# Performance work log

Hardware: AMD Instinct MI355X
Metric: run time of the kernel (lower is better)

The kernel has to match this reference:

```python
import jax, jax.numpy as jnp
import numpy as np

B, T = 256, 128
DW = 768          # dim_word
DH = 768          # dim_hidden (must equal DW per broadcast in original code)
NC = 3            # num_classification
VOCAB = 50000
TVOCAB = 5000


def setup_inputs() -> dict:
    key = jax.random.key(0)
    ks = jax.random.split(key, 16)
    u = 1.0 / np.sqrt(DH)
    uni = lambda k, shape: jax.random.uniform(k, shape, jnp.float32, -u, u)
    inp = {
        'sent': jax.random.randint(ks[0], (B, T), 0, VOCAB),
        'target': jax.random.randint(ks[1], (B,), 0, TVOCAB),
        'lens': jnp.clip(jax.random.randint(ks[2], (B,), 0, T + 1), 1, T),
        'emb': jax.random.normal(ks[3], (VOCAB, DW), jnp.float32) * 0.1,
        'temb': jax.random.normal(ks[4], (TVOCAB, DW), jnp.float32) * 0.1,
        # LSTM cell params: input = cat(x_t, target_x) -> 2*DW
        'W_ih': uni(ks[5], (2 * DW, 4 * DH)),
        'W_hh': uni(ks[6], (DH, 4 * DH)),
        'b_lstm': uni(ks[7], (4 * DH,)),
        'Wh': uni(ks[8], (DH, DH)),
        'Wv': uni(ks[9], (DW, DW)),
        'w': uni(ks[10], (DH + DW,)),
        'Wp': uni(ks[11], (DH, DH)),
        'Wx': uni(ks[12], (DH, DH)),
        'W_lin': uni(ks[13], (DH, NC)),
        'b_lin': uni(ks[14], (NC,)),
    }
    return inp


def _forward(sent, target, lens, emb, temb, W_ih, W_hh, b_lstm, Wh, Wv, w, Wp, Wx, W_lin, b_lin):
    x = emb[sent]                      # [B, T, DW]
    tx = temb[target]                  # [B, DW]
    mask = (jnp.arange(T)[None, :] < lens[:, None]).astype(x.dtype)  # [B, T]

    def step(carry, ins):
        h, c = carry
        xt, mt = ins                   # [B, DW], [B]
        inp = jnp.concatenate([xt, tx], axis=-1)          # [B, 2*DW]
        gates = inp @ W_ih + h @ W_hh + b_lstm            # [B, 4*DH]
        i, f, g, o = jnp.split(gates, 4, axis=-1)
        c_new = jax.nn.sigmoid(f) * c + jax.nn.sigmoid(i) * jnp.tanh(g)
        h_new = jax.nn.sigmoid(o) * jnp.tanh(c_new)
        m = mt[:, None]
        h = m * h_new + (1.0 - m) * h   # mask blend (hold state past seq end)
        c = m * c_new + (1.0 - m) * c
        return (h, c), h

    h0 = jnp.zeros((x.shape[0], DH), x.dtype)
    c0 = jnp.zeros((x.shape[0], DH), x.dtype)
    xs = (jnp.swapaxes(x, 0, 1), mask.T)                 # time-major
    _, Hs = jax.lax.scan(step, (h0, c0), xs)
    H = jnp.swapaxes(Hs, 0, 1)                            # [B, T, DH]

    # attention: M = tanh([H Wh ; aspect Wv]); scores = M @ w, masked softmax
    aspect_proj = (tx @ Wv)[:, None, :]                   # [B, 1, DW] broadcast over T
    M = jnp.tanh(jnp.concatenate(
        [H @ Wh, jnp.broadcast_to(aspect_proj, H.shape)], axis=-1))  # [B, T, DH+DW]
    scores = M @ w                                        # [B, T]
    scores = jnp.where(mask > 0, scores, -1e9)
    alpha = jax.nn.softmax(scores, axis=-1)               # [B, T]
    r = jnp.einsum('bt,btd->bd', alpha, H)                # [B, DH]
    h_star = jnp.tanh(r @ Wp + H[:, -1, :] @ Wx)          # [B, DH]
    # dropout is identity in eval mode
    logit = h_star @ W_lin + b_lin                        # [B, NC]
    return logit


def reference(sent, target, lens, emb, temb, W_ih, W_hh, b_lstm, Wh, Wv, w, Wp, Wx, W_lin, b_lin):
    return _forward(sent, target, lens, emb, temb, W_ih, W_hh, b_lstm,
                    Wh, Wv, w, Wp, Wx, W_lin, b_lin)
```

## Files before the change

kernel.cpp:

```cpp
#include <hip/hip_runtime.h>
#include <stdint.h>

#define Bz 256
#define Tz 128
#define DWz 768
#define DHz 768
#define G4z 3072
#define NBLK 96
#define NGRID 256
#define VOCABz 50000

typedef __attribute__((ext_vector_type(8))) short short8;
typedef __attribute__((ext_vector_type(4))) float f32x4;
typedef __attribute__((ext_vector_type(4))) int i32x4;

__device__ __forceinline__ unsigned short f2bf(float x) {
    union { float f; unsigned int u; } v; v.f = x;
    unsigned int u = v.u;
    return (unsigned short)((u + 0x7fffu + ((u >> 16) & 1u)) >> 16);
}
__device__ __forceinline__ float bf2f(unsigned short h) {
    union { unsigned int u; float f; } v; v.u = ((unsigned int)h) << 16;
    return v.f;
}
__device__ __forceinline__ float fsigm(float x) {
    return __builtin_amdgcn_rcpf(1.0f + __builtin_amdgcn_exp2f(x * -1.4426950408889634f));
}
__device__ __forceinline__ float ftanh(float x) {
    x = fminf(fmaxf(x, -15.0f), 15.0f);
    float e = __builtin_amdgcn_exp2f(x * -2.8853900817779268f);
    return (1.0f - e) * __builtin_amdgcn_rcpf(1.0f + e);
}

__global__ void k_cvt4(const float* __restrict__ src, unsigned short* __restrict__ dst, int n4) {
    int i = blockIdx.x * blockDim.x + threadIdx.x;
    int st = gridDim.x * blockDim.x;
    for (; i < n4; i += st) {
        float4 v = ((const float4*)src)[i];
        ushort4 o;
        o.x = f2bf(v.x); o.y = f2bf(v.y); o.z = f2bf(v.z); o.w = f2bf(v.w);
        ((ushort4*)dst)[i] = o;
    }
}

__global__ void k_prep_tx(const int* __restrict__ target, const float* __restrict__ temb,
                          float* __restrict__ tx) {
    int b = blockIdx.x;
    long row = (long)target[b] * DWz;
    for (int d = threadIdx.x; d < DWz; d += blockDim.x)
        tx[b * DWz + d] = temb[row + d];
}

__global__ __launch_bounds__(256) void k_prep_wswz(const float* __restrict__ W,
                                                   unsigned short* __restrict__ out, int NT) {
    __shared__ float sT[32][132];
    int bid = blockIdx.x;
    int kt = bid / NT, nt = bid - kt * NT;
    int tid = threadIdx.x;
    int ldn = NT * 128;
    {
        int r = tid >> 3;
        int cb = (tid & 7) * 16;
        const float* src = W + (long)(kt * 32 + r) * ldn + nt * 128 + cb;
#pragma unroll
        for (int u = 0; u < 4; ++u) {
            float4 v = ((const float4*)src)[u];
            sT[r][cb + u * 4 + 0] = v.x; sT[r][cb + u * 4 + 1] = v.y;
            sT[r][cb + u * 4 + 2] = v.z; sT[r][cb + u * 4 + 3] = v.w;
        }
    }
    __syncthreads();
#pragma unroll
    for (int it = 0; it < 2; ++it) {
        int s = tid + it * 256;
        int n = s >> 2, kq = s & 3;
        alignas(16) unsigned short o[8];
#pragma unroll
        for (int e = 0; e < 8; ++e) o[e] = f2bf(sT[kq * 8 + e][n]);
        *(int4*)(out + ((long)bid * 512 + s) * 8) = *(const int4*)o;
    }
}

__global__ __launch_bounds__(256) void k_prep_whh(const float* __restrict__ Whh,
                                                  unsigned short* __restrict__ WhhP) {
    __shared__ float sT[32][65];
    int bid = blockIdx.x;
    int dblk = bid / 24;
    int k0c = bid - dblk * 24;
    int tid = threadIdx.x;
    {
        int kk = tid >> 3;
        int seg = tid & 7;
        const float* src = Whh + (long)(k0c * 32 + kk) * G4z
                         + (seg >> 1) * 768 + dblk * 16 + (seg & 1) * 8;
        float4 v0 = *(const float4*)src;
        float4 v1 = *(const float4*)(src + 4);
        int cl = seg * 8;
        sT[kk][cl + 0] = v0.x; sT[kk][cl + 1] = v0.y; sT[kk][cl + 2] = v0.z; sT[kk][cl + 3] = v0.w;
        sT[kk][cl + 4] = v1.x; sT[kk][cl + 5] = v1.y; sT[kk][cl + 6] = v1.z; sT[kk][cl + 7] = v1.w;
    }
    __syncthreads();
    {
        int nl = tid >> 2, cc = tid & 3;
        int q8 = cc ^ ((nl >> 1) & 3);
        int clv = (nl >> 4) * 16 + (nl & 15);
        alignas(16) unsigned short o[8];
#pragma unroll
        for (int e = 0; e < 8; ++e) o[e] = f2bf(sT[q8 * 8 + e][clv]);
        *(int4*)(WhhP + (long)(dblk * 6144 + k0c * 256 + tid) * 8) = *(const int4*)o;
    }
}

__global__ void k_gemm_f32_bias(const float* __restrict__ A, const float* __restrict__ Bm,
                                const float* __restrict__ bias, float* __restrict__ C,
                                int M, int N, int K, int lda, int ldb) {
    __shared__ float sA[16][65];
    __shared__ float sB[16][65];
    int bn = blockIdx.x * 64, bm = blockIdx.y * 64;
    int tx = threadIdx.x & 15, ty = threadIdx.x >> 4;
    float acc[4][4] = {};
    for (int k0 = 0; k0 < K; k0 += 16) {
        for (int l = threadIdx.x; l < 64 * 16; l += 256) {
            int m = l >> 4, k = l & 15;
            sA[k][m] = A[(long)(bm + m) * lda + k0 + k];
        }
        for (int l = threadIdx.x; l < 16 * 64; l += 256) {
            int k = l >> 6, n = l & 63;
            sB[k][n] = Bm[(long)(k0 + k) * ldb + bn + n];
        }
        __syncthreads();
        for (int k = 0; k < 16; ++k) {
            float a0[4], b0[4];
#pragma unroll
            for (int i = 0; i < 4; ++i) a0[i] = sA[k][ty * 4 + i];
#pragma unroll
            for (int j = 0; j < 4; ++j) b0[j] = sB[k][tx * 4 + j];
#pragma unroll
            for (int i = 0; i < 4; ++i)
#pragma unroll
                for (int j = 0; j < 4; ++j) acc[i][j] += a0[i] * b0[j];
        }
        __syncthreads();
    }
#pragma unroll
    for (int i = 0; i < 4; ++i)
#pragma unroll
        for (int j = 0; j < 4; ++j) {
            int m = bm + ty * 4 + i, n = bn + tx * 4 + j;
            C[(long)m * N + n] = acc[i][j] + bias[n];
        }
}

__global__ __launch_bounds__(256) void k_gemm_x(const float* __restrict__ emb,
                                                const unsigned short* __restrict__ embb,
                                                int ebb,
                                                const int* __restrict__ sent,
                                                const unsigned short* __restrict__ WbP,
                                                unsigned short* __restrict__ xW) {
    __shared__ unsigned short sA[128 * 40];
    __shared__ unsigned short sB[128 * 40];
    int tid = threadIdx.x;
    int n0 = blockIdx.x * 128;
    int m0 = blockIdx.y * 128;
    int wid = tid >> 6, lane = tid & 63, l15 = lane & 15, q = lane >> 4;
    int wm = wid >> 1, wn = wid & 1;
    int arow = tid >> 1;
    int kp = (tid & 1) * 16;
    int m = m0 + arow;
    int tt = m >> 8;
    int bb = m & 255;
    long gbase = (long)sent[bb * Tz + tt] * DWz;
    int s0 = tid, s1 = tid + 256;
    int bd0 = (s0 >> 2) * 40 + (((s0 & 3) ^ (((s0 >> 2) >> 3) & 3)) << 3);
    int bd1 = (s1 >> 2) * 40 + (((s1 & 3) ^ (((s1 >> 2) >> 3) & 3)) << 3);

    f32x4 acc[4][4];
    f32x4 zz = {0.f, 0.f, 0.f, 0.f};
#pragma unroll
    for (int i = 0; i < 4; ++i)
#pragma unroll
        for (int j = 0; j < 4; ++j) acc[i][j] = zz;

    for (int k0 = 0; k0 < DWz; k0 += 32) {
        if (ebb) {
            const unsigned short* src = embb + gbase + k0 + kp;
            *(int4*)(sA + arow * 40 + kp) = *(const int4*)src;
            *(int4*)(sA + arow * 40 + kp + 8) = *(const int4*)(src + 8);
        } else {
            const float* src = emb + gbase + k0 + kp;
            alignas(16) unsigned short tmp[16];
#pragma unroll
            for (int it = 0; it < 4; ++it) {
                float4 v = ((const float4*)src)[it];
                tmp[it * 4 + 0] = f2bf(v.x); tmp[it * 4 + 1] = f2bf(v.y);
                tmp[it * 4 + 2] = f2bf(v.z); tmp[it * 4 + 3] = f2bf(v.w);
            }
            *(int4*)(sA + arow * 40 + kp) = *(const int4*)tmp;
            *(int4*)(sA + arow * 40 + kp + 8) = *(const int4*)(tmp + 8);
        }
        {
            const int4* wsrc = (const int4*)WbP
                + ((long)((k0 >> 5) * 24 + (n0 >> 7))) * 512 + tid;
            int4 v0 = wsrc[0];
            int4 v1 = wsrc[256];
            *(int4*)(sB + bd0) = v0;
            *(int4*)(sB + bd1) = v1;
        }
        __syncthreads();
        short8 af[4], bfr[4];
#pragma unroll
        for (int i = 0; i < 4; ++i)
            af[i] = *(const short8*)(sA + (wm * 64 + i * 16 + l15) * 40 + q * 8);
#pragma unroll
        for (int j = 0; j < 4; ++j) {
            int n = wn * 64 + j * 16 + l15;
            bfr[j] = *(const short8*)(sB + n * 40 + ((q ^ ((n >> 3) & 3)) << 3));
        }
#pragma unroll
        for (int i = 0; i < 4; ++i)
#pragma unroll
            for (int j = 0; j < 4; ++j)
                acc[i][j] = __builtin_amdgcn_mfma_f32_16x16x32_bf16(af[i], bfr[j], acc[i][j], 0, 0, 0);
        __syncthreads();
    }
#pragma unroll
    for (int j = 0; j < 4; ++j) {
        int n = n0 + wn * 64 + j * 16 + l15;
        int gt = n / 768;
        int dblk = (n - gt * 768) >> 4;
#pragma unroll
        for (int ip = 0; ip < 2; ++ip) {
            int row = m0 + wm * 64 + ip * 32;
            int t = row >> 8;
            int bq = (row & 255) + q * 4;
            int blk = dblk * 2 + (bq >> 7);
            int tidd = ((bq & 127) >> 5) * 64 + q * 16 + l15;
            alignas(16) unsigned short o[8];
#pragma unroll
            for (int r = 0; r < 4; ++r) {
                o[r]     = f2bf(acc[ip * 2][j][r]);
                o[4 + r] = f2bf(acc[ip * 2 + 1][j][r]);
            }
            *(int4*)(xW + (((long)t * 96 + blk) * 4 + gt) * 2048 + (long)tidd * 8) = *(const int4*)o;
        }
    }
}

#define UNPACK(PF, G)                                                        \
    {                                                                        \
        const unsigned short* ch_ = (const unsigned short*)&(PF);            \
        _Pragma("unroll")                                                    \
        for (int i_ = 0; i_ < 2; ++i_)                                       \
            _Pragma("unroll")                                                \
            for (int r_ = 0; r_ < 4; ++r_)                                   \
                xg[i_][G][r_] = bf2f(ch_[i_ * 4 + r_]) + xgc[i_][G][r_];     \
    }

__global__ __launch_bounds__(256, 1) void k_lstm_all(int t0, int t1,
        unsigned short* __restrict__ xW, const float* __restrict__ constg,
        const unsigned short* __restrict__ WhhP, unsigned short* __restrict__ Hbf,
        float* __restrict__ cbuf, const int* __restrict__ lens,
        unsigned* __restrict__ bar, unsigned* __restrict__ xwcnt, int waitxw,
        const float* __restrict__ emb, const unsigned short* __restrict__ embb,
        int ebb, const int* __restrict__ sent,
        const unsigned short* __restrict__ WihbP, int nprod) {
    extern __shared__ unsigned short sB[];
    int bid = blockIdx.x;
    int tid = threadIdx.x;
    int lane = tid & 63, wid = tid >> 6;
    int l15 = lane & 15, q = lane >> 4;

    if (bid >= NBLK) {
        unsigned short* psA = sB;
        unsigned short* psB = sB + 5120;
        int wm = wid >> 1, wn = wid & 1;
        int arow = tid >> 1;
        int kp = (tid & 1) * 16;
        int s0 = tid, s1 = tid + 256;
        int bd0 = (s0 >> 2) * 40 + (((s0 & 3) ^ (((s0 >> 2) >> 3) & 3)) << 3);
        int bd1 = (s1 >> 2) * 40 + (((s1 & 3) ^ (((s1 >> 2) >> 3) & 3)) << 3);

        for (int g = bid - NBLK; g < 6144; g += nprod) {
            int my = g / 24, nx = g - (g / 24) * 24;
            int m0 = my * 128, n0 = nx * 128;
            int m = m0 + arow;
            int tt = m >> 8, bb2 = m & 255;
            long gbase = (long)sent[bb2 * Tz + tt] * DWz;

            f32x4 acc[4][4];
            f32x4 zz = {0.f, 0.f, 0.f, 0.f};
#pragma unroll
            for (int i = 0; i < 4; ++i)
#pragma unroll
                for (int j = 0; j < 4; ++j) acc[i][j] = zz;

            for (int k0 = 0; k0 < DWz; k0 += 32) {
                if (ebb) {
                    const unsigned short* src = embb + gbase + k0 + kp;
                    *(int4*)(psA + arow * 40 + kp) = *(const int4*)src;
                    *(int4*)(psA + arow * 40 + kp + 8) = *(const int4*)(src + 8);
                } else {
                    const float* src = emb + gbase + k0 + kp;
                    alignas(16) unsigned short tmp[16];
#pragma unroll
                    for (int it = 0; it < 4; ++it) {
                        float4 v = ((const float4*)src)[it];
                        tmp[it * 4 + 0] = f2bf(v.x); tmp[it * 4 + 1] = f2bf(v.y);
                        tmp[it * 4 + 2] = f2bf(v.z); tmp[it * 4 + 3] = f2bf(v.w);
                    }
                    *(int4*)(psA + arow * 40 + kp) = *(const int4*)tmp;
                    *(int4*)(psA + arow * 40 + kp + 8) = *(const int4*)(tmp + 8);
                }
                {
                    const int4* wsrc = (const int4*)WihbP
                        + ((long)((k0 >> 5) * 24 + (n0 >> 7))) * 512 + tid;
                    int4 v0 = wsrc[0];
                    int4 v1 = wsrc[256];
                    *(int4*)(psB + bd0) = v0;
                    *(int4*)(psB + bd1) = v1;
                }
                __syncthreads();
                short8 af[4], bfr[4];
#pragma unroll
                for (int i = 0; i < 4; ++i)
                    af[i] = *(const short8*)(psA + (wm * 64 + i * 16 + l15) * 40 + q * 8);
#pragma unroll
                for (int j = 0; j < 4; ++j) {
                    int n = wn * 64 + j * 16 + l15;
                    bfr[j] = *(const short8*)(psB + n * 40 + ((q ^ ((n >> 3) & 3)) << 3));
                }
#pragma unroll
                for (int i = 0; i < 4; ++i)
#pragma unroll
                    for (int j = 0; j < 4; ++j)
                        acc[i][j] = __builtin_amdgcn_mfma_f32_16x16x32_bf16(af[i], bfr[j], acc[i][j], 0, 0, 0);
                __syncthreads();
            }
#pragma unroll
            for (int j = 0; j < 4; ++j) {
                int n = n0 + wn * 64 + j * 16 + l15;
                int gt = n / 768;
                int dblk2 = (n - gt * 768) >> 4;
#pragma unroll
                for (int ip = 0; ip < 2; ++ip) {
                    int row = m0 + wm * 64 + ip * 32;
                    int t = row >> 8;
                    int bq = (row & 255) + q * 4;
                    int blk = dblk2 * 2 + (bq >> 7);
                    int tidd = ((bq & 127) >> 5) * 64 + q * 16 + l15;
                    alignas(16) unsigned short o[8];
#pragma unroll
                    for (int r = 0; r < 4; ++r) {
                        o[r]     = f2bf(acc[ip * 2][j][r]);
                        o[4 + r] = f2bf(acc[ip * 2 + 1][j][r]);
                    }
                    unsigned long long* dst = (unsigned long long*)
                        (xW + (((long)t * 96 + blk) * 4 + gt) * 2048 + (long)tidd * 8);
                    const unsigned long long* po = (const unsigned long long*)o;
                    __hip_atomic_store(dst, po[0], __ATOMIC_RELAXED, __HIP_MEMORY_SCOPE_AGENT);
                    __hip_atomic_store(dst + 1, po[1], __ATOMIC_RELAXED, __HIP_MEMORY_SCOPE_AGENT);
                }
            }
            asm volatile("s_waitcnt vmcnt(0)" ::: "memory");
            __syncthreads();
            if (tid == 0)
                (void)__hip_atomic_fetch_add(&xwcnt[(my >> 1) * 32], 1u,
                                             __ATOMIC_RELAXED, __HIP_MEMORY_SCOPE_AGENT);
        }
        return;
    }

    int bm = bid & 1;
    int dblk = bid >> 1;
    int d0 = dblk * 16;
    int d = d0 + l15;
    unsigned* flg = bar + ((bm * 4 + wid) * 48) * 32;

    {
        const int4* src = (const int4*)WhhP + (long)dblk * 6144;
        for (int s = tid; s < 6144; s += 256) ((int4*)sB)[s] = src[s];
    }

    int brow[8];
    int lenr[8];
    float c[8], h[8];
    float xgc[2][4][4];
#pragma unroll
    for (int i = 0; i < 2; ++i)
#pragma unroll
        for (int r = 0; r < 4; ++r) {
            int ir = i * 4 + r;
            int b = bm * 128 + wid * 32 + i * 16 + q * 4 + r;
            brow[ir] = b;
            lenr[ir] = lens[b];
            long cbase = (long)b * G4z + d;
#pragma unroll
            for (int j = 0; j < 4; ++j) xgc[i][j][r] = constg[cbase + j * 768];
            if (t0 > 0) {
                c[ir] = cbuf[(long)b * DHz + d];
                h[ir] = bf2f(Hbf[((long)b * Tz + (t0 - 1)) * DHz + d]);
            } else { c[ir] = 0.f; h[ir] = 0.f; }
        }

    int bbase[4];
#pragma unroll
    for (int j = 0; j < 4; ++j) {
        int nl = j * 16 + l15;
        bbase[j] = nl * 32 + ((q ^ ((nl >> 1) & 3)) << 3);
    }
    __syncthreads();

    if (waitxw) {
        const unsigned* xc = xwcnt + t0 * 32;
        if (lane == 0)
            while (__hip_atomic_load(xc, __ATOMIC_RELAXED, __HIP_MEMORY_SCOPE_AGENT) < 48u)
                __builtin_amdgcn_s_sleep(1);
        asm volatile("" ::: "memory");
    }
    float xg[2][4][4];
    {
        const unsigned short* x0 = xW + ((long)t0 * 96 + bid) * 8192 + (long)tid * 8;
        int4 c0 = *(const int4*)(x0);
        int4 c1 = *(const int4*)(x0 + 2048);
        int4 c2 = *(const int4*)(x0 + 4096);
        int4 c3 = *(const int4*)(x0 + 6144);
        UNPACK(c0, 0) UNPACK(c1, 1) UNPACK(c2, 2) UNPACK(c3, 3)
    }

    i32x4 pf0, pf1, pf2, pf3;

    for (int t = t0; t < t1; ++t) {
        if (t > t0) {
            unsigned tgt = (unsigned)t;
            const unsigned* fp = flg + lane * 32;
            while (true) {
                unsigned v = (lane < 48)
                    ? __hip_atomic_load(fp, __ATOMIC_RELAXED, __HIP_MEMORY_SCOPE_AGENT)
                    : tgt;
                if (__all(v >= tgt)) break;
                __builtin_amdgcn_s_sleep(1);
            }
            asm volatile("s_waitcnt vmcnt(0)" ::: "memory");
            __builtin_amdgcn_sched_barrier(0);
            UNPACK(pf0, 0) UNPACK(pf1, 1) UNPACK(pf2, 2) UNPACK(pf3, 3)
        }

        f32x4 acc[2][4];
        f32x4 zz = {0.f, 0.f, 0.f, 0.f};
#pragma unroll
        for (int i = 0; i < 2; ++i)
#pragma unroll
            for (int j = 0; j < 4; ++j) acc[i][j] = zz;

        if (t > 0) {
            const unsigned short* ap0 = Hbf + ((long)(bm * 128 + wid * 32 + l15) * Tz + (t - 1)) * DHz + q * 8;
            const unsigned short* ap1 = ap0 + (long)16 * Tz * DHz;
#pragma unroll 6
            for (int k0c = 0; k0c < 24; ++k0c) {
                short8 a0 = *(const short8*)(ap0 + k0c * 32);
                short8 a1 = *(const short8*)(ap1 + k0c * 32);
                const unsigned short* bb = sB + k0c * 2048;
#pragma unroll
                for (int j = 0; j < 4; ++j) {
                    short8 bf = *(const short8*)(bb + bbase[j]);
                    acc[0][j] = __builtin_amdgcn_mfma_f32_16x16x32_bf16(a0, bf, acc[0][j], 0, 0, 0);
                    acc[1][j] = __builtin_amdgcn_mfma_f32_16x16x32_bf16(a1, bf, acc[1][j], 0, 0, 0);
                }
            }
        }

#pragma unroll
        for (int i = 0; i < 2; ++i)
#pragma unroll
            for (int r = 0; r < 4; ++r) {
                int ir = i * 4 + r;
                float gi = acc[i][0][r] + xg[i][0][r];
                float gf = acc[i][1][r] + xg[i][1][r];
                float gg = acc[i][2][r] + xg[i][2][r];
                float go = acc[i][3][r] + xg[i][3][r];
                float cn = fsigm(gf) * c[ir] + fsigm(gi) * ftanh(gg);
                float hn = fsigm(go) * ftanh(cn);
                bool upd = t < lenr[ir];
                c[ir] = upd ? cn : c[ir];
                h[ir] = upd ? hn : h[ir];
                __hip_atomic_store(Hbf + ((long)brow[ir] * Tz + t) * DHz + d, f2bf(h[ir]),
                                   __ATOMIC_RELAXED, __HIP_MEMORY_SCOPE_AGENT);
            }

        if (t + 1 < t1) {
            if (waitxw) {
                const unsigned* xc = xwcnt + (t + 1) * 32;
                if (lane == 0)
                    while (__hip_atomic_load(xc, __ATOMIC_RELAXED, __HIP_MEMORY_SCOPE_AGENT) < 48u)
                        __builtin_amdgcn_s_sleep(1);
                asm volatile("" ::: "memory");
            }
            const unsigned short* pp = xW + ((long)(t + 1) * 96 + bid) * 8192 + (long)tid * 8;
            asm volatile(
                "global_load_dwordx4 %0, %4, off\n\t"
                "global_load_dwordx4 %1, %5, off\n\t"
                "global_load_dwordx4 %2, %6, off\n\t"
                "global_load_dwordx4 %3, %7, off"
                : "=&v"(pf0), "=&v"(pf1), "=&v"(pf2), "=&v"(pf3)
                : "v"(pp), "v"(pp + 2048), "v"(pp + 4096), "v"(pp + 6144)
                : "memory");
            asm volatile("s_waitcnt vmcnt(4)" ::: "memory");
            if (lane == 0)
                __hip_atomic_store(flg + dblk * 32, (unsigned)(t + 1),
                                   __ATOMIC_RELAXED, __HIP_MEMORY_SCOPE_AGENT);
        }
    }
#pragma unroll
    for (int ir = 0; ir < 8; ++ir) cbuf[(long)brow[ir] * DHz + d] = c[ir];
}

__global__ __launch_bounds__(256) void k_scores(const unsigned short* __restrict__ Hbf,
                                                const unsigned short* __restrict__ WbP,
                                                const float* __restrict__ wv,
                                                float* __restrict__ scores) {
    __shared__ unsigned short sA[128 * 40];
    __shared__ unsigned short sB[128 * 40];
    __shared__ float sred[128];
    int tid = threadIdx.x;
    int n0 = blockIdx.x * 128;
    int m0 = blockIdx.y * 128;
    int wid = tid >> 6, lane = tid & 63, l15 = lane & 15, q = lane >> 4;
    int wm = wid >> 1, wn = wid & 1;

    int s0 = tid, s1 = tid + 256;
    int bd0 = (s0 >> 2) * 40 + (((s0 & 3) ^ (((s0 >> 2) >> 3) & 3)) << 3);
    int bd1 = (s1 >> 2) * 40 + (((s1 & 3) ^ (((s1 >> 2) >> 3) & 3)) << 3);

    f32x4 acc[4][4];
    f32x4 zz = {0.f, 0.f, 0.f, 0.f};
#pragma unroll
    for (int i = 0; i < 4; ++i)
#pragma unroll
        for (int j = 0; j < 4; ++j) acc[i][j] = zz;

    int arow = tid >> 1;
    int kp = (tid & 1) * 16;
    const unsigned short* asrc = Hbf + (long)(m0 + arow) * DHz;

    for (int k0 = 0; k0 < DHz; k0 += 32) {
        *(int4*)(sA + arow * 40 + kp) = *(const int4*)(asrc + k0 + kp);
        *(int4*)(sA + arow * 40 + kp + 8) = *(const int4*)(asrc + k0 + kp + 8);
        {
            const int4* wsrc = (const int4*)WbP
                + ((long)((k0 >> 5) * 6 + (n0 >> 7))) * 512 + tid;
            int4 v0 = wsrc[0];
            int4 v1 = wsrc[256];
            *(int4*)(sB + bd0) = v0;
            *(int4*)(sB + bd1) = v1;
        }
        __syncthreads();
        short8 af[4], bfr[4];
#pragma unroll
        for (int i = 0; i < 4; ++i)
            af[i] = *(const short8*)(sA + (wm * 64 + i * 16 + l15) * 40 + q * 8);
#pragma unroll
        for (int j = 0; j < 4; ++j) {
            int n = wn * 64 + j * 16 + l15;
            bfr[j] = *(const short8*)(sB + n * 40 + ((q ^ ((n >> 3) & 3)) << 3));
        }
#pragma unroll
        for (int i = 0; i < 4; ++i)
#pragma unroll
            for (int j = 0; j < 4; ++j)
                acc[i][j] = __builtin_amdgcn_mfma_f32_16x16x32_bf16(af[i], bfr[j], acc[i][j], 0, 0, 0);
        __syncthreads();
    }
    if (tid < 128) sred[tid] = 0.f;
    __syncthreads();
#pragma unroll
    for (int i = 0; i < 4; ++i)
#pragma unroll
        for (int r = 0; r < 4; ++r) {
            float sv = 0.f;
#pragma unroll
            for (int j = 0; j < 4; ++j) {
                int n = n0 + wn * 64 + j * 16 + l15;
                sv += ftanh(acc[i][j][r]) * wv[n];
            }
#pragma unroll
            for (int o = 1; o < 16; o <<= 1) sv += __shfl_xor(sv, o, 64);
            if (l15 == 0) atomicAdd(&sred[wm * 64 + i * 16 + q * 4 + r], sv);
        }
    __syncthreads();
    if (tid < 128) atomicAdd(&scores[m0 + tid], sred[tid]);
}

__global__ void k_softmax(const float* __restrict__ scores, const int* __restrict__ lens,
                          float* __restrict__ alpha) {
    int b = blockIdx.x, t = threadIdx.x;
    int len = lens[b];
    float s = (t < len) ? scores[b * Tz + t] : -1e9f;
    float m = s;
#pragma unroll
    for (int o = 32; o; o >>= 1) m = fmaxf(m, __shfl_xor(m, o, 64));
    __shared__ float rA[2], rB[2];
    if ((t & 63) == 0) rA[t >> 6] = m;
    __syncthreads();
    m = fmaxf(rA[0], rA[1]);
    float e = expf(s - m);
    float sum = e;
#pragma unroll
    for (int o = 32; o; o >>= 1) sum += __shfl_xor(sum, o, 64);
    if ((t & 63) == 0) rB[t >> 6] = sum;
    __syncthreads();
    sum = rB[0] + rB[1];
    alpha[b * Tz + t] = e / sum;
}

__global__ __launch_bounds__(128) void k_r(const float* __restrict__ alpha,
                                           const unsigned short* __restrict__ Hbf,
                                           float* __restrict__ rbuf) {
    int b = blockIdx.x;
    int tid = threadIdx.x;
    __shared__ float sal[Tz];
    if (tid < Tz) sal[tid] = alpha[b * Tz + tid];
    __syncthreads();
    if (tid < 96) {
        const unsigned short* hp = Hbf + (long)b * Tz * DHz + tid * 8;
        float acc[8] = {};
        for (int t = 0; t < Tz; ++t) {
            short8 v = *(const short8*)(hp + (long)t * DHz);
            float a = sal[t];
            const unsigned short* pv = (const unsigned short*)&v;
#pragma unroll
            for (int e = 0; e < 8; ++e) acc[e] += a * bf2f(pv[e]);
        }
        float* rp = rbuf + (long)b * DHz + tid * 8;
#pragma unroll
        for (int e = 0; e < 8; ++e) rp[e] = acc[e];
    }
}

__global__ void k_hstar(const float* __restrict__ rbuf, const unsigned short* __restrict__ Hbf,
                        const float* __restrict__ Wp, const float* __restrict__ Wx,
                        float* __restrict__ hst) {
    __shared__ float sA[16][65];
    __shared__ float sB[16][65];
    int bn = blockIdx.x * 64, bm = blockIdx.y * 64;
    int tx = threadIdx.x & 15, ty = threadIdx.x >> 4;
    float acc[4][4] = {};
    for (int src = 0; src < 2; ++src) {
        const float* Bm = src ? Wx : Wp;
        for (int k0 = 0; k0 < DHz; k0 += 16) {
            for (int l = threadIdx.x; l < 64 * 16; l += 256) {
                int mm = l >> 4, kk = l & 15;
                sA[kk][mm] = src ? bf2f(Hbf[((long)(bm + mm) * Tz + (Tz - 1)) * DHz + k0 + kk])
                                 : rbuf[(long)(bm + mm) * DHz + k0 + kk];
            }
            for (int l = threadIdx.x; l < 16 * 64; l += 256) {
                int kk = l >> 6, nn = l & 63;
                sB[kk][nn] = Bm[(long)(k0 + kk) * DHz + bn + nn];
            }
            __syncthreads();
            for (int k = 0; k < 16; ++k) {
                float a0[4], b0[4];
#pragma unroll
                for (int i = 0; i < 4; ++i) a0[i] = sA[k][ty * 4 + i];
#pragma unroll
                for (int j = 0; j < 4; ++j) b0[j] = sB[k][tx * 4 + j];
#pragma unroll
                for (int i = 0; i < 4; ++i)
#pragma unroll
                    for (int j = 0; j < 4; ++j) acc[i][j] += a0[i] * b0[j];
            }
            __syncthreads();
        }
    }
#pragma unroll
    for (int i = 0; i < 4; ++i)
#pragma unroll
        for (int j = 0; j < 4; ++j)
            hst[(long)(bm + ty * 4 + i) * DHz + bn + tx * 4 + j] = ftanh(acc[i][j]);
}

__global__ void k_logits(const float* __restrict__ hst, const float* __restrict__ Wl,
                         const float* __restrict__ bl, float* __restrict__ out) {
    int b = blockIdx.x;
    int lane = threadIdx.x & 63, c = threadIdx.x >> 6;
    float s = 0.f;
    for (int k = lane; k < DHz; k += 64) s += hst[(long)b * DHz + k] * Wl[k * 3 + c];
#pragma unroll
    for (int o = 32; o; o >>= 1) s += __shfl_xor(s, o, 64);
    if (lane == 0) out[b * 3 + c] = s + bl[c];
}

extern "C" void kernel_launch(void* const* d_in, const int* in_sizes, int n_in,
                              void* d_out, int out_size, void* d_ws, size_t ws_size,
                              hipStream_t stream) {
    (void)in_sizes; (void)n_in; (void)out_size;
    const int*   sent   = (const int*)d_in[0];
    const int*   target = (const int*)d_in[1];
    const int*   lens   = (const int*)d_in[2];
    const float* emb    = (const float*)d_in[3];
    const float* temb   = (const float*)d_in[4];
    const float* W_ih   = (const float*)d_in[5];
    const float* W_hh   = (const float*)d_in[6];
    const float* b_lstm = (const float*)d_in[7];
    const float* Wh     = (const float*)d_in[8];
    const float* wv     = (const float*)d_in[10];
    const float* Wp     = (const float*)d_in[11];
    const float* Wx     = (const float*)d_in[12];
    const float* W_lin  = (const float*)d_in[13];
    const float* b_lin  = (const float*)d_in[14];
    float* out = (float*)d_out;

    char* ws = (char*)d_ws;
    size_t off = 0;
    auto alloc = [&](size_t bytes) -> void* {
        void* p = ws + off;
        off = (off + bytes + 255) & ~(size_t)255;
        return p;
    };
    unsigned short* xW    = (unsigned short*)alloc((size_t)32768 * G4z * 2);
    unsigned short* Hbf   = (unsigned short*)alloc((size_t)Bz * Tz * DHz * 2);
    unsigned short* WihbP = (unsigned short*)alloc((size_t)24 * 24 * 512 * 16);
    unsigned short* WhhP  = (unsigned short*)alloc((size_t)48 * 6144 * 16);
    unsigned short* WhbP  = (unsigned short*)alloc((size_t)24 * 6 * 512 * 16);
    float* tx     = (float*)alloc((size_t)Bz * DWz * 4);
    float* constg = (float*)alloc((size_t)Bz * G4z * 4);
    float* cbuf   = (float*)alloc((size_t)Bz * DHz * 4);
    float* scores = (float*)alloc((size_t)Bz * Tz * 4);
    float* alpha  = (float*)alloc((size_t)Bz * Tz * 4);
    float* rbuf   = (float*)alloc((size_t)Bz * DHz * 4);
    float* hst    = (float*)alloc((size_t)Bz * DHz * 4);
    unsigned* bar = (unsigned*)alloc(65536);
    unsigned* xwc = (unsigned*)alloc(16384);

    size_t embb_bytes = (size_t)VOCABz * DWz * 2;
    unsigned short* embb = (unsigned short*)alloc(embb_bytes);
    int ebb = (off <= ws_size) ? 1 : 0;

    if (ebb) k_cvt4<<<4096, 256, 0, stream>>>(emb, embb, VOCABz * DWz / 4);
    k_prep_wswz<<<576, 256, 0, stream>>>(W_ih, WihbP, 24);
    k_prep_wswz<<<144, 256, 0, stream>>>(Wh, WhbP, 6);
    k_prep_whh<<<1152, 256, 0, stream>>>(W_hh, WhhP);
    k_prep_tx<<<Bz, 256, 0, stream>>>(target, temb, tx);
    hipMemsetAsync(scores, 0, (size_t)Bz * Tz * 4, stream);
    hipMemsetAsync(bar, 0, 65536, stream);
    hipMemsetAsync(xwc, 0, 16384, stream);

    k_gemm_f32_bias<<<dim3(48, 4), 256, 0, stream>>>(tx, W_ih + (size_t)DWz * G4z, b_lstm,
                                                     constg, Bz, G4z, DWz, DWz, G4z);

    hipFuncSetAttribute((const void*)k_lstm_all,
                        hipFuncAttributeMaxDynamicSharedMemorySize, 98304);
    int t0v = 0, t1v = Tz, waitv = 1, nprodv = NGRID - NBLK;
    unsigned short* xWp = xW;
    const float* cgp = constg;
    const unsigned short* whp = WhhP;
    unsigned short* hbp = Hbf;
    float* cbp = cbuf;
    const int* lnp = lens;
    unsigned* barp = bar;
    unsigned* xwcp = xwc;
    const float* embp = emb;
    const unsigned short* embbp = embb;
    const int* sentp = sent;
    const unsigned short* wihp = WihbP;
    void* kargs[] = {&t0v, &t1v, &xWp, &cgp, &whp, &hbp, &cbp, &lnp, &barp,
                     &xwcp, &waitv, &embp, &embbp, &ebb, &sentp, &wihp, &nprodv};
    hipError_t ce = hipLaunchCooperativeKernel(reinterpret_cast<void*>(k_lstm_all),
                                               dim3(NGRID), dim3(256), kargs, 98304, stream);
    if (ce != hipSuccess) {
        k_gemm_x<<<dim3(24, 256), 256, 0, stream>>>(emb, embb, ebb, sent, WihbP, xW);
        for (int t = 0; t < Tz; ++t)
            k_lstm_all<<<NBLK, 256, 98304, stream>>>(t, t + 1, xW, constg, WhhP, Hbf,
                                                     cbuf, lens, bar, xwc, 0,
                                                     emb, embb, ebb, sent, WihbP, 0);
    }

    k_scores<<<dim3(6, 256), 256, 0, stream>>>(Hbf, WhbP, wv, scores);
    k_softmax<<<Bz, 128, 0, stream>>>(scores, lens, alpha);
    k_r<<<Bz, 128, 0, stream>>>(alpha, Hbf, rbuf);
    k_hstar<<<dim3(12, 4), 256, 0, stream>>>(rbuf, Hbf, Wp, Wx, hst);
    k_logits<<<Bz, 192, 0, stream>>>(hst, W_lin, b_lin, out);
}
```

Before: 2.320 ms.

## Drop bf16 embedding pre-conversion; move small GEMMs to MFMA; fuse softmax with context

Removes the full-vocabulary fp32-to-bf16 conversion of the embedding table, so the LSTM producer path now converts only the gathered rows on the fly. The target-constant gate GEMM and the h_star GEMM are rewritten as bf16 MFMA tiled kernels over pre-swizzled weights, replacing scalar fp32 SIMT GEMMs. Softmax and the alpha-weighted sum of H are fused into one kernel, and the tx gather is folded into the GEMM. The cost is extra weight-prep launches and bf16 rounding in GEMMs that were previously fp32.

```diff
diff --git a/kernel.cpp b/kernel.cpp
--- a/kernel.cpp
+++ b/kernel.cpp
@@ -8,7 +8,6 @@
 #define G4z 3072
 #define NBLK 96
 #define NGRID 256
-#define VOCABz 50000
 
 typedef __attribute__((ext_vector_type(8))) short short8;
 typedef __attribute__((ext_vector_type(4))) float f32x4;
@@ -30,25 +29,6 @@
     x = fminf(fmaxf(x, -15.0f), 15.0f);
     float e = __builtin_amdgcn_exp2f(x * -2.8853900817779268f);
     return (1.0f - e) * __builtin_amdgcn_rcpf(1.0f + e);
-}
-
-__global__ void k_cvt4(const float* __restrict__ src, unsigned short* __restrict__ dst, int n4) {
-    int i = blockIdx.x * blockDim.x + threadIdx.x;
-    int st = gridDim.x * blockDim.x;
-    for (; i < n4; i += st) {
-        float4 v = ((const float4*)src)[i];
-        ushort4 o;
-        o.x = f2bf(v.x); o.y = f2bf(v.y); o.z = f2bf(v.z); o.w = f2bf(v.w);
-        ((ushort4*)dst)[i] = o;
-    }
-}
-
-__global__ void k_prep_tx(const int* __restrict__ target, const float* __restrict__ temb,
-                          float* __restrict__ tx) {
-    int b = blockIdx.x;
-    long row = (long)target[b] * DWz;
-    for (int d = threadIdx.x; d < DWz; d += blockDim.x)
-        tx[b * DWz + d] = temb[row + d];
 }
 
 __global__ __launch_bounds__(256) void k_prep_wswz(const float* __restrict__ W,
@@ -111,49 +91,85 @@
     }
 }
 
-__global__ void k_gemm_f32_bias(const float* __restrict__ A, const float* __restrict__ Bm,
-                                const float* __restrict__ bias, float* __restrict__ C,
-                                int M, int N, int K, int lda, int ldb) {
-    __shared__ float sA[16][65];
-    __shared__ float sB[16][65];
-    int bn = blockIdx.x * 64, bm = blockIdx.y * 64;
-    int tx = threadIdx.x & 15, ty = threadIdx.x >> 4;
-    float acc[4][4] = {};
-    for (int k0 = 0; k0 < K; k0 += 16) {
-        for (int l = threadIdx.x; l < 64 * 16; l += 256) {
-            int m = l >> 4, k = l & 15;
-            sA[k][m] = A[(long)(bm + m) * lda + k0 + k];
-        }
-        for (int l = threadIdx.x; l < 16 * 64; l += 256) {
-            int k = l >> 6, n = l & 63;
-            sB[k][n] = Bm[(long)(k0 + k) * ldb + bn + n];
+__global__ __launch_bounds__(256) void k_gemm_cg(const int* __restrict__ target,
+                                                 const float* __restrict__ temb,
+                                                 const unsigned short* __restrict__ WbP,
+                                                 const float* __restrict__ bias,
+                                                 float* __restrict__ C) {
+    __shared__ unsigned short sA[128 * 40];
+    __shared__ unsigned short sB[128 * 40];
+    int tid = threadIdx.x;
+    int n0 = blockIdx.x * 128;
+    int m0 = blockIdx.y * 128;
+    int wid = tid >> 6, lane = tid & 63, l15 = lane & 15, q = lane >> 4;
+    int wm = wid >> 1, wn = wid & 1;
+    int arow = tid >> 1;
+    int kp = (tid & 1) * 16;
+    long gbase = (long)target[m0 + arow] * DWz;
+    int s0 = tid, s1 = tid + 256;
+    int bd0 = (s0 >> 2) * 40 + (((s0 & 3) ^ (((s0 >> 2) >> 3) & 3)) << 3);
+    int bd1 = (s1 >> 2) * 40 + (((s1 & 3) ^ (((s1 >> 2) >> 3) & 3)) << 3);
+
+    f32x4 acc[4][4];
+    f32x4 zz = {0.f, 0.f, 0.f, 0.f};
+#pragma unroll
+    for (int i = 0; i < 4; ++i)
+#pragma unroll
+        for (int j = 0; j < 4; ++j) acc[i][j] = zz;
+
+    for (int k0 = 0; k0 < DWz; k0 += 32) {
+        {
+            const float* src = temb + gbase + k0 + kp;
+            alignas(16) unsigned short tmp[16];
+#pragma unroll
+            for (int it = 0; it < 4; ++it) {
+                float4 v = ((const float4*)src)[it];
+                tmp[it * 4 + 0] = f2bf(v.x); tmp[it * 4 + 1] = f2bf(v.y);
+                tmp[it * 4 + 2] = f2bf(v.z); tmp[it * 4 + 3] = f2bf(v.w);
+            }
+            *(int4*)(sA + arow * 40 + kp) = *(const int4*)tmp;
+            *(int4*)(sA + arow * 40 + kp + 8) = *(const int4*)(tmp + 8);
+        }
+        {
+            const int4* wsrc = (const int4*)WbP
+                + ((long)((k0 >> 5) * 24 + (n0 >> 7))) * 512 + tid;
+            int4 v0 = wsrc[0];
+            int4 v1 = wsrc[256];
+            *(int4*)(sB + bd0) = v0;
+            *(int4*)(sB + bd1) = v1;
         }
         __syncthreads();
-        for (int k = 0; k < 16; ++k) {
-            float a0[4], b0[4];
-#pragma unroll
-            for (int i = 0; i < 4; ++i) a0[i] = sA[k][ty * 4 + i];
-#pragma unroll
-            for (int j = 0; j < 4; ++j) b0[j] = sB[k][tx * 4 + j];
-#pragma unroll
-            for (int i = 0; i < 4; ++i)
-#pragma unroll
-                for (int j = 0; j < 4; ++j) acc[i][j] += a0[i] * b0[j];
-        }
+        short8 af[4], bfr[4];
+#pragma unroll
+        for (int i = 0; i < 4; ++i)
+            af[i] = *(const short8*)(sA + (wm * 64 + i * 16 + l15) * 40 + q * 8);
+#pragma unroll
+        for (int j = 0; j < 4; ++j) {
+            int n = wn * 64 + j * 16 + l15;
+            bfr[j] = *(const short8*)(sB + n * 40 + ((q ^ ((n >> 3) & 3)) << 3));
+        }
+#pragma unroll
+        for (int i = 0; i < 4; ++i)
+#pragma unroll
+            for (int j = 0; j < 4; ++j)
+                acc[i][j] = __builtin_amdgcn_mfma_f32_16x16x32_bf16(af[i], bfr[j], acc[i][j], 0, 0, 0);
         __syncthreads();
     }
 #pragma unroll
     for (int i = 0; i < 4; ++i)
 #pragma unroll
         for (int j = 0; j < 4; ++j) {
-            int m = bm + ty * 4 + i, n = bn + tx * 4 + j;
-            C[(long)m * N + n] = acc[i][j] + bias[n];
+            int col = n0 + wn * 64 + j * 16 + l15;
+            float bv = bias[col];
+#pragma unroll
+            for (int r = 0; r < 4; ++r) {
+                int row = m0 + wm * 64 + i * 16 + q * 4 + r;
+                C[(long)row * G4z + col] = acc[i][j][r] + bv;
+            }
         }
 }
 
 __global__ __launch_bounds__(256) void k_gemm_x(const float* __restrict__ emb,
-                                                const unsigned short* __restrict__ embb,
-                                                int ebb,
                                                 const int* __restrict__ sent,
                                                 const unsigned short* __restrict__ WbP,
                                                 unsigned short* __restrict__ xW) {
@@ -182,11 +198,7 @@
         for (int j = 0; j < 4; ++j) acc[i][j] = zz;
 
     for (int k0 = 0; k0 < DWz; k0 += 32) {
-        if (ebb) {
-            const unsigned short* src = embb + gbase + k0 + kp;
-            *(int4*)(sA + arow * 40 + kp) = *(const int4*)src;
-            *(int4*)(sA + arow * 40 + kp + 8) = *(const int4*)(src + 8);
-        } else {
+        {
             const float* src = emb + gbase + k0 + kp;
             alignas(16) unsigned short tmp[16];
 #pragma unroll
@@ -261,8 +273,7 @@
         const unsigned short* __restrict__ WhhP, unsigned short* __restrict__ Hbf,
         float* __restrict__ cbuf, const int* __restrict__ lens,
         unsigned* __restrict__ bar, unsigned* __restrict__ xwcnt, int waitxw,
-        const float* __restrict__ emb, const unsigned short* __restrict__ embb,
-        int ebb, const int* __restrict__ sent,
+        const float* __restrict__ emb, const int* __restrict__ sent,
         const unsigned short* __restrict__ WihbP, int nprod) {
     extern __shared__ unsigned short sB[];
     int bid = blockIdx.x;
@@ -295,11 +306,7 @@
                 for (int j = 0; j < 4; ++j) acc[i][j] = zz;
 
             for (int k0 = 0; k0 < DWz; k0 += 32) {
-                if (ebb) {
-                    const unsigned short* src = embb + gbase + k0 + kp;
-                    *(int4*)(psA + arow * 40 + kp) = *(const int4*)src;
-                    *(int4*)(psA + arow * 40 + kp + 8) = *(const int4*)(src + 8);
-                } else {
+                {
                     const float* src = emb + gbase + k0 + kp;
                     alignas(16) unsigned short tmp[16];
 #pragma unroll
@@ -590,15 +597,18 @@
     if (tid < 128) atomicAdd(&scores[m0 + tid], sred[tid]);
 }
 
-__global__ void k_softmax(const float* __restrict__ scores, const int* __restrict__ lens,
-                          float* __restrict__ alpha) {
+__global__ __launch_bounds__(128) void k_attn(const float* __restrict__ scores,
+                                              const int* __restrict__ lens,
+                                              const unsigned short* __restrict__ Hbf,
+                                              float* __restrict__ rbuf) {
     int b = blockIdx.x, t = threadIdx.x;
+    __shared__ float sal[Tz];
+    __shared__ float rA[2], rB[2];
     int len = lens[b];
     float s = (t < len) ? scores[b * Tz + t] : -1e9f;
     float m = s;
 #pragma unroll
     for (int o = 32; o; o >>= 1) m = fmaxf(m, __shfl_xor(m, o, 64));
-    __shared__ float rA[2], rB[2];
     if ((t & 63) == 0) rA[t >> 6] = m;
     __syncthreads();
     m = fmaxf(rA[0], rA[1]);
@@ -609,73 +619,102 @@
     if ((t & 63) == 0) rB[t >> 6] = sum;
     __syncthreads();
     sum = rB[0] + rB[1];
-    alpha[b * Tz + t] = e / sum;
-}
-
-__global__ __launch_bounds__(128) void k_r(const float* __restrict__ alpha,
-                                           const unsigned short* __restrict__ Hbf,
-                                           float* __restrict__ rbuf) {
-    int b = blockIdx.x;
+    sal[t] = e / sum;
+    __syncthreads();
+    if (t < 96) {
+        const unsigned short* hp = Hbf + (long)b * Tz * DHz + t * 8;
+        float acc[8] = {};
+        for (int tt = 0; tt < Tz; ++tt) {
+            short8 v = *(const short8*)(hp + (long)tt * DHz);
+            float a = sal[tt];
+            const unsigned short* pv = (const unsigned short*)&v;
+#pragma unroll
+            for (int e2 = 0; e2 < 8; ++e2) acc[e2] += a * bf2f(pv[e2]);
+        }
+        float* rp = rbuf + (long)b * DHz + t * 8;
+#pragma unroll
+        for (int e2 = 0; e2 < 8; ++e2) rp[e2] = acc[e2];
+    }
+}
+
+__global__ __launch_bounds__(256) void k_hstar(const float* __restrict__ rbuf,
+                                               const unsigned short* __restrict__ Hbf,
+                                               const unsigned short* __restrict__ WbP,
+                                               float* __restrict__ hst) {
+    __shared__ unsigned short sA[128 * 40];
+    __shared__ unsigned short sB[128 * 40];
     int tid = threadIdx.x;
-    __shared__ float sal[Tz];
-    if (tid < Tz) sal[tid] = alpha[b * Tz + tid];
-    __syncthreads();
-    if (tid < 96) {
-        const unsigned short* hp = Hbf + (long)b * Tz * DHz + tid * 8;
-        float acc[8] = {};
-        for (int t = 0; t < Tz; ++t) {
-            short8 v = *(const short8*)(hp + (long)t * DHz);
-            float a = sal[t];
-            const unsigned short* pv = (const unsigned short*)&v;
-#pragma unroll
-            for (int e = 0; e < 8; ++e) acc[e] += a * bf2f(pv[e]);
-        }
-        float* rp = rbuf + (long)b * DHz + tid * 8;
-#pragma unroll
-        for (int e = 0; e < 8; ++e) rp[e] = acc[e];
-    }
-}
-
-__global__ void k_hstar(const float* __restrict__ rbuf, const unsigned short* __restrict__ Hbf,
-                        const float* __restrict__ Wp, const float* __restrict__ Wx,
-                        float* __restrict__ hst) {
-    __shared__ float sA[16][65];
-    __shared__ float sB[16][65];
-    int bn = blockIdx.x * 64, bm = blockIdx.y * 64;
-    int tx = threadIdx.x & 15, ty = threadIdx.x >> 4;
-    float acc[4][4] = {};
-    for (int src = 0; src < 2; ++src) {
-        const float* Bm = src ? Wx : Wp;
-        for (int k0 = 0; k0 < DHz; k0 += 16) {
-            for (int l = threadIdx.x; l < 64 * 16; l += 256) {
-                int mm = l >> 4, kk = l & 15;
-                sA[kk][mm] = src ? bf2f(Hbf[((long)(bm + mm) * Tz + (Tz - 1)) * DHz + k0 + kk])
-                                 : rbuf[(long)(bm + mm) * DHz + k0 + kk];
-            }
-            for (int l = threadIdx.x; l < 16 * 64; l += 256) {
-                int kk = l >> 6, nn = l & 63;
-                sB[kk][nn] = Bm[(long)(k0 + kk) * DHz + bn + nn];
-            }
-            __syncthreads();
-            for (int k = 0; k < 16; ++k) {
-                float a0[4], b0[4];
-#pragma unroll
-                for (int i = 0; i < 4; ++i) a0[i] = sA[k][ty * 4 + i];
-#pragma unroll
-                for (int j = 0; j < 4; ++j) b0[j] = sB[k][tx * 4 + j];
-#pragma unroll
-                for (int i = 0; i < 4; ++i)
-#pragma unroll
-                    for (int j = 0; j < 4; ++j) acc[i][j] += a0[i] * b0[j];
-            }
-            __syncthreads();
-        }
-    }
+    int n0 = blockIdx.x * 128;
+    int m0 = blockIdx.y * 128;
+    int wid = tid >> 6, lane = tid & 63, l15 = lane & 15, q = lane >> 4;
+    int wm = wid >> 1, wn = wid & 1;
+    int arow = tid >> 1;
+    int kp = (tid & 1) * 16;
+    int s0 = tid, s1 = tid + 256;
+    int bd0 = (s0 >> 2) * 40 + (((s0 & 3) ^ (((s0 >> 2) >> 3) & 3)) << 3);
+    int bd1 = (s1 >> 2) * 40 + (((s1 & 3) ^ (((s1 >> 2) >> 3) & 3)) << 3);
+
+    f32x4 acc[4][4];
+    f32x4 zz = {0.f, 0.f, 0.f, 0.f};
 #pragma unroll
     for (int i = 0; i < 4; ++i)
 #pragma unroll
-        for (int j = 0; j < 4; ++j)
-            hst[(long)(bm + ty * 4 + i) * DHz + bn + tx * 4 + j] = ftanh(acc[i][j]);
+        for (int j = 0; j < 4; ++j) acc[i][j] = zz;
+
+    for (int k0 = 0; k0 < 2 * DHz; k0 += 32) {
+        if (k0 < DHz) {
+            const float* src = rbuf + (long)(m0 + arow) * DHz + k0 + kp;
+            alignas(16) unsigned short tmp[16];
+#pragma unroll
+            for (int it = 0; it < 4; ++it) {
+                float4 v = ((const float4*)src)[it];
+                tmp[it * 4 + 0] = f2bf(v.x); tmp[it * 4 + 1] = f2bf(v.y);
+                tmp[it * 4 + 2] = f2bf(v.z); tmp[it * 4 + 3] = f2bf(v.w);
+            }
+            *(int4*)(sA + arow * 40 + kp) = *(const int4*)tmp;
+            *(int4*)(sA + arow * 40 + kp + 8) = *(const int4*)(tmp + 8);
+        } else {
+            const unsigned short* src = Hbf + ((long)(m0 + arow) * Tz + (Tz - 1)) * DHz
+                                      + (k0 - DHz) + kp;
+            *(int4*)(sA + arow * 40 + kp) = *(const int4*)src;
+            *(int4*)(sA + arow * 40 + kp + 8) = *(const int4*)(src + 8);
+        }
+        {
+            const int4* wsrc = (const int4*)WbP
+                + ((long)((k0 >> 5) * 6 + (n0 >> 7))) * 512 + tid;
+            int4 v0 = wsrc[0];
+            int4 v1 = wsrc[256];
+            *(int4*)(sB + bd0) = v0;
+            *(int4*)(sB + bd1) = v1;
+        }
+        __syncthreads();
+        short8 af[4], bfr[4];
+#pragma unroll
+        for (int i = 0; i < 4; ++i)
+            af[i] = *(const short8*)(sA + (wm * 64 + i * 16 + l15) * 40 + q * 8);
+#pragma unroll
+        for (int j = 0; j < 4; ++j) {
+            int n = wn * 64 + j * 16 + l15;
+            bfr[j] = *(const short8*)(sB + n * 40 + ((q ^ ((n >> 3) & 3)) << 3));
+        }
+#pragma unroll
+        for (int i = 0; i < 4; ++i)
+#pragma unroll
+            for (int j = 0; j < 4; ++j)
+                acc[i][j] = __builtin_amdgcn_mfma_f32_16x16x32_bf16(af[i], bfr[j], acc[i][j], 0, 0, 0);
+        __syncthreads();
+    }
+#pragma unroll
+    for (int i = 0; i < 4; ++i)
+#pragma unroll
+        for (int j = 0; j < 4; ++j) {
+            int col = n0 + wn * 64 + j * 16 + l15;
+#pragma unroll
+            for (int r = 0; r < 4; ++r) {
+                int row = m0 + wm * 64 + i * 16 + q * 4 + r;
+                hst[(long)row * DHz + col] = ftanh(acc[i][j][r]);
+            }
+        }
 }
 
 __global__ void k_logits(const float* __restrict__ hst, const float* __restrict__ Wl,
@@ -692,7 +731,7 @@
 extern "C" void kernel_launch(void* const* d_in, const int* in_sizes, int n_in,
                               void* d_out, int out_size, void* d_ws, size_t ws_size,
                               hipStream_t stream) {
-    (void)in_sizes; (void)n_in; (void)out_size;
+    (void)in_sizes; (void)n_in; (void)out_size; (void)ws_size;
     const int*   sent   = (const int*)d_in[0];
     const int*   target = (const int*)d_in[1];
     const int*   lens   = (const int*)d_in[2];
@@ -719,33 +758,29 @@
     unsigned short* xW    = (unsigned short*)alloc((size_t)32768 * G4z * 2);
     unsigned short* Hbf   = (unsigned short*)alloc((size_t)Bz * Tz * DHz * 2);
     unsigned short* WihbP = (unsigned short*)alloc((size_t)24 * 24 * 512 * 16);
+    unsigned short* Wih2P = (unsigned short*)alloc((size_t)24 * 24 * 512 * 16);
     unsigned short* WhhP  = (unsigned short*)alloc((size_t)48 * 6144 * 16);
     unsigned short* WhbP  = (unsigned short*)alloc((size_t)24 * 6 * 512 * 16);
-    float* tx     = (float*)alloc((size_t)Bz * DWz * 4);
+    unsigned short* WpxP  = (unsigned short*)alloc((size_t)48 * 6 * 512 * 16);
     float* constg = (float*)alloc((size_t)Bz * G4z * 4);
     float* cbuf   = (float*)alloc((size_t)Bz * DHz * 4);
     float* scores = (float*)alloc((size_t)Bz * Tz * 4);
-    float* alpha  = (float*)alloc((size_t)Bz * Tz * 4);
     float* rbuf   = (float*)alloc((size_t)Bz * DHz * 4);
     float* hst    = (float*)alloc((size_t)Bz * DHz * 4);
     unsigned* bar = (unsigned*)alloc(65536);
     unsigned* xwc = (unsigned*)alloc(16384);
 
-    size_t embb_bytes = (size_t)VOCABz * DWz * 2;
-    unsigned short* embb = (unsigned short*)alloc(embb_bytes);
-    int ebb = (off <= ws_size) ? 1 : 0;
-
-    if (ebb) k_cvt4<<<4096, 256, 0, stream>>>(emb, embb, VOCABz * DWz / 4);
     k_prep_wswz<<<576, 256, 0, stream>>>(W_ih, WihbP, 24);
+    k_prep_wswz<<<576, 256, 0, stream>>>(W_ih + (size_t)DWz * G4z, Wih2P, 24);
     k_prep_wswz<<<144, 256, 0, stream>>>(Wh, WhbP, 6);
+    k_prep_wswz<<<144, 256, 0, stream>>>(Wp, WpxP, 6);
+    k_prep_wswz<<<144, 256, 0, stream>>>(Wx, WpxP + (size_t)144 * 512 * 8, 6);
     k_prep_whh<<<1152, 256, 0, stream>>>(W_hh, WhhP);
-    k_prep_tx<<<Bz, 256, 0, stream>>>(target, temb, tx);
     hipMemsetAsync(scores, 0, (size_t)Bz * Tz * 4, stream);
     hipMemsetAsync(bar, 0, 65536, stream);
     hipMemsetAsync(xwc, 0, 16384, stream);
 
-    k_gemm_f32_bias<<<dim3(48, 4), 256, 0, stream>>>(tx, W_ih + (size_t)DWz * G4z, b_lstm,
-                                                     constg, Bz, G4z, DWz, DWz, G4z);
+    k_gemm_cg<<<dim3(24, 2), 256, 0, stream>>>(target, temb, Wih2P, b_lstm, constg);
 
     hipFuncSetAttribute((const void*)k_lstm_all,
                         hipFuncAttributeMaxDynamicSharedMemorySize, 98304);
@@ -759,24 +794,22 @@
     unsigned* barp = bar;
     unsigned* xwcp = xwc;
     const float* embp = emb;
-    const unsigned short* embbp = embb;
     const int* sentp = sent;
     const unsigned short* wihp = WihbP;
     void* kargs[] = {&t0v, &t1v, &xWp, &cgp, &whp, &hbp, &cbp, &lnp, &barp,
-                     &xwcp, &waitv, &embp, &embbp, &ebb, &sentp, &wihp, &nprodv};
+                     &xwcp, &waitv, &embp, &sentp, &wihp, &nprodv};
     hipError_t ce = hipLaunchCooperativeKernel(reinterpret_cast<void*>(k_lstm_all),
                                                dim3(NGRID), dim3(256), kargs, 98304, stream);
     if (ce != hipSuccess) {
-        k_gemm_x<<<dim3(24, 256), 256, 0, stream>>>(emb, embb, ebb, sent, WihbP, xW);
+        k_gemm_x<<<dim3(24, 256), 256, 0, stream>>>(emb, sent, WihbP, xW);
         for (int t = 0; t < Tz; ++t)
             k_lstm_all<<<NBLK, 256, 98304, stream>>>(t, t + 1, xW, constg, WhhP, Hbf,
                                                      cbuf, lens, bar, xwc, 0,
-                                                     emb, embb, ebb, sent, WihbP, 0);
+                                                     emb, sent, WihbP, 0);
     }
 
     k_scores<<<dim3(6, 256), 256, 0, stream>>>(Hbf, WhbP, wv, scores);
-    k_softmax<<<Bz, 128, 0, stream>>>(scores, lens, alpha);
-    k_r<<<Bz, 128, 0, stream>>>(alpha, Hbf, rbuf);
-    k_hstar<<<dim3(12, 4), 256, 0, stream>>>(rbuf, Hbf, Wp, Wx, hst);
+    k_attn<<<Bz, 128, 0, stream>>>(scores, lens, Hbf, rbuf);
+    k_hstar<<<dim3(6, 2), 256, 0, stream>>>(rbuf, Hbf, WpxP, hst);
     k_logits<<<Bz, 192, 0, stream>>>(hst, W_lin, b_lin, out);
 }
```

After: 1.909 ms. 17.7% less time.
